# Kernel tuning notes

Measured on AMD Instinct MI355X. Metric: run time of the kernel, lower is better.

## Reference

```python
import jax, jax.numpy as jnp
import numpy as np

B = 4194304  # batch rows
DX = 10      # input feature dim (hardcoded in module)
DH = 4       # hidden dim (hardcoded in module)


def setup_inputs() -> dict:
    key = jax.random.key(0)
    ks = jax.random.split(key, 14)
    s_in = 1.0 / np.sqrt(DX)
    s_h = 1.0 / np.sqrt(DH)
    return {
        "x": jax.random.normal(ks[0], (B, DX), jnp.float32),
        "hidden": jax.random.normal(ks[1], (B, DH), jnp.float32),
        # torch.nn.Linear weights: W has shape [out, in], y = x @ W.T + b
        "Wzh": jax.random.uniform(ks[2], (DH, DH), jnp.float32, -s_h, s_h),
        "bzh": jax.random.uniform(ks[3], (DH,), jnp.float32, -s_h, s_h),
        "Wzx": jax.random.uniform(ks[4], (DH, DX), jnp.float32, -s_in, s_in),
        "bzx": jax.random.uniform(ks[5], (DH,), jnp.float32, -s_in, s_in),
        "Wrh": jax.random.uniform(ks[6], (DH, DH), jnp.float32, -s_h, s_h),
        "brh": jax.random.uniform(ks[7], (DH,), jnp.float32, -s_h, s_h),
        "Wrx": jax.random.uniform(ks[8], (DH, DX), jnp.float32, -s_in, s_in),
        "brx": jax.random.uniform(ks[9], (DH,), jnp.float32, -s_in, s_in),
        "Wnx": jax.random.uniform(ks[10], (DH, DX), jnp.float32, -s_in, s_in),
        "bnx": jax.random.uniform(ks[11], (DH,), jnp.float32, -s_in, s_in),
        "Wnh": jax.random.uniform(ks[12], (DH, DH), jnp.float32, -s_h, s_h),
        "bnh": jax.random.uniform(ks[13], (DH,), jnp.float32, -s_h, s_h),
    }


def reference(x, hidden, Wzh, bzh, Wzx, bzx, Wrh, brh, Wrx, brx, Wnx, bnx, Wnh, bnh):
    # z = sigmoid(hidden @ Wzh.T + bzh + x @ Wzx.T + bzx)
    z = jax.nn.sigmoid(hidden @ Wzh.T + bzh + x @ Wzx.T + bzx)
    r = jax.nn.sigmoid(hidden @ Wrh.T + brh + x @ Wrx.T + brx)
    n = jnp.tanh(r * (hidden @ Wnh.T + bnh) + x @ Wnx.T + bnx)
    return (1.0 - z) * n + z * hidden
```

## Files before the change

kernel.cpp:

```cpp
#include <hip/hip_runtime.h>
#include <math.h>


constexpr int DXc = 10;
constexpr int DHc = 4;

__global__ __launch_bounds__(256, 4)
void gru_fused(const float* __restrict__ x,
               const float* __restrict__ hidden,
               const float* __restrict__ Wzh, const float* __restrict__ bzh,
               const float* __restrict__ Wzx, const float* __restrict__ bzx,
               const float* __restrict__ Wrh, const float* __restrict__ brh,
               const float* __restrict__ Wrx, const float* __restrict__ brx,
               const float* __restrict__ Wnx, const float* __restrict__ bnx,
               const float* __restrict__ Wnh, const float* __restrict__ bnh,
               float* __restrict__ out, int total )
{
    const int tid = blockIdx.x * blockDim.x + threadIdx.x;
    const int nth = gridDim.x * blockDim.x;
    const int j   = tid & 3;

    float wzh[DHc], wrh[DHc], wnh[DHc];
    float wzx[DXc], wrx[DXc], wnx[DXc];
#pragma unroll
    for (int k = 0; k < DHc; ++k) {
        wzh[k] = Wzh[j * DHc + k];
        wrh[k] = Wrh[j * DHc + k];
        wnh[k] = Wnh[j * DHc + k];
    }
#pragma unroll
    for (int k = 0; k < DXc; ++k) {
        wzx[k] = Wzx[j * DXc + k];
        wrx[k] = Wrx[j * DXc + k];
        wnx[k] = Wnx[j * DXc + k];
    }
    const float bz    = bzh[j] + bzx[j];
    const float br    = brh[j] + brx[j];
    const float bnh_j = bnh[j];
    const float bnx_j = bnx[j];

    for (int p = tid; p < total; p += nth) {
        const int row = p >> 2;

        const float2* xr = reinterpret_cast<const float2*>(x + row * DXc);
        float xv[DXc];
#pragma unroll
        for (int q = 0; q < DXc / 2; ++q) {
            const float2 t = xr[q];
            xv[2 * q]     = t.x;
            xv[2 * q + 1] = t.y;
        }
        const float4 hv = *reinterpret_cast<const float4*>(hidden + row * DHc);
        const float hvv[DHc] = {hv.x, hv.y, hv.z, hv.w};

        float az = bz, ar = br, ah = bnh_j, ax = bnx_j;
#pragma unroll
        for (int k = 0; k < DHc; ++k) {
            az = fmaf(hvv[k], wzh[k], az);
            ar = fmaf(hvv[k], wrh[k], ar);
            ah = fmaf(hvv[k], wnh[k], ah);
        }
#pragma unroll
        for (int k = 0; k < DXc; ++k) {
            az = fmaf(xv[k], wzx[k], az);
            ar = fmaf(xv[k], wrx[k], ar);
            ax = fmaf(xv[k], wnx[k], ax);
        }

        const float z = 1.0f / (1.0f + expf(-az));
        const float r = 1.0f / (1.0f + expf(-ar));
        const float n = tanhf(fmaf(r, ah, ax));

        const float hj = (j < 2) ? (j == 0 ? hv.x : hv.y)
                                 : (j == 2 ? hv.z : hv.w);

        out[p] = fmaf(z, hj - n, n);
    }
}

extern "C" void kernel_launch(void* const* d_in, const int* in_sizes, int n_in,
                              void* d_out, int out_size, void* d_ws, size_t ws_size,
                              hipStream_t stream) {
    const float* x   = (const float*)d_in[0];
    const float* h   = (const float*)d_in[1];
    const float* Wzh = (const float*)d_in[2];
    const float* bzh = (const float*)d_in[3];
    const float* Wzx = (const float*)d_in[4];
    const float* bzx = (const float*)d_in[5];
    const float* Wrh = (const float*)d_in[6];
    const float* brh = (const float*)d_in[7];
    const float* Wrx = (const float*)d_in[8];
    const float* brx = (const float*)d_in[9];
    const float* Wnx = (const float*)d_in[10];
    const float* bnx = (const float*)d_in[11];
    const float* Wnh = (const float*)d_in[12];
    const float* bnh = (const float*)d_in[13];
    float* out = (float*)d_out;

    const int total = out_size;
    const int block = 256;
    const int grid  = 2048;

    gru_fused<<<grid, block, 0, stream>>>(x, h, Wzh, bzh, Wzx, bzx,
                                          Wrh, brh, Wrx, brx,
                                          Wnx, bnx, Wnh, bnh, out, total);
}
```

Baseline: 335.6 us.

## Assign one output column per wavefront with scalar weights and LDS-transposed stores

Each wavefront of a block now handles a single output column j for 64 consecutive rows. This lets all weights and biases live in scalar registers via readfirstlane, instead of every thread holding its own copy. The outputs pass through a double-buffered shared-memory transpose (with a swizzle to avoid bank conflicts) so the global store stays coalesced. Exact expf/tanhf are replaced with fast exp and hardware reciprocal, and the occupancy hint in launch bounds is raised. In exchange there is a barrier every iteration, and each row's x/hidden is now loaded by four wavefronts, relying on cache to absorb the repeats.

Result: faster. 326.5 us (-2.7%).

```diff
diff --git a/kernel.cpp b/kernel.cpp
--- a/kernel.cpp
+++ b/kernel.cpp
@@ -5,7 +5,11 @@
 constexpr int DXc = 10;
 constexpr int DHc = 4;
 
-__global__ __launch_bounds__(256, 4)
+__device__ __forceinline__ float sgpr_f(float v) {
+    return __uint_as_float(__builtin_amdgcn_readfirstlane(__float_as_uint(v)));
+}
+
+__global__ __launch_bounds__(256, 8)
 void gru_fused(const float* __restrict__ x,
                const float* __restrict__ hidden,
                const float* __restrict__ Wzh, const float* __restrict__ bzh,
@@ -14,43 +18,45 @@
                const float* __restrict__ Wrx, const float* __restrict__ brx,
                const float* __restrict__ Wnx, const float* __restrict__ bnx,
                const float* __restrict__ Wnh, const float* __restrict__ bnh,
-               float* __restrict__ out, int total )
+               float* __restrict__ out, int nrows)
 {
-    const int tid = blockIdx.x * blockDim.x + threadIdx.x;
-    const int nth = gridDim.x * blockDim.x;
-    const int j   = tid & 3;
+    __shared__ float obuf[2 * 256];
+
+    const int tid  = threadIdx.x;
+    const int lane = tid & 63;
+    const int j    = __builtin_amdgcn_readfirstlane(tid >> 6);
 
     float wzh[DHc], wrh[DHc], wnh[DHc];
     float wzx[DXc], wrx[DXc], wnx[DXc];
 #pragma unroll
     for (int k = 0; k < DHc; ++k) {
-        wzh[k] = Wzh[j * DHc + k];
-        wrh[k] = Wrh[j * DHc + k];
-        wnh[k] = Wnh[j * DHc + k];
+        wzh[k] = sgpr_f(Wzh[j * DHc + k]);
+        wrh[k] = sgpr_f(Wrh[j * DHc + k]);
+        wnh[k] = sgpr_f(Wnh[j * DHc + k]);
     }
 #pragma unroll
     for (int k = 0; k < DXc; ++k) {
-        wzx[k] = Wzx[j * DXc + k];
-        wrx[k] = Wrx[j * DXc + k];
-        wnx[k] = Wnx[j * DXc + k];
+        wzx[k] = sgpr_f(Wzx[j * DXc + k]);
+        wrx[k] = sgpr_f(Wrx[j * DXc + k]);
+        wnx[k] = sgpr_f(Wnx[j * DXc + k]);
     }
-    const float bz    = bzh[j] + bzx[j];
-    const float br    = brh[j] + brx[j];
-    const float bnh_j = bnh[j];
-    const float bnx_j = bnx[j];
+    const float bz    = sgpr_f(bzh[j] + bzx[j]);
+    const float br    = sgpr_f(brh[j] + brx[j]);
+    const float bnh_j = sgpr_f(bnh[j]);
+    const float bnx_j = sgpr_f(bnx[j]);
 
-    for (int p = tid; p < total; p += nth) {
-        const int row = p >> 2;
+    int widx = (lane << 2) | ((j + (lane >> 3)) & 3);
+    int ridx = (tid & ~3) | (((tid & 3) + (tid >> 5)) & 3);
+
+    const int rstride = gridDim.x * 64;
+    for (int row0 = blockIdx.x * 64; row0 < nrows; row0 += rstride) {
+        const int row = row0 + lane;
 
         const float2* xr = reinterpret_cast<const float2*>(x + row * DXc);
-        float xv[DXc];
-#pragma unroll
-        for (int q = 0; q < DXc / 2; ++q) {
-            const float2 t = xr[q];
-            xv[2 * q]     = t.x;
-            xv[2 * q + 1] = t.y;
-        }
+        const float2 x0 = xr[0], x1 = xr[1], x2 = xr[2], x3 = xr[3], x4 = xr[4];
         const float4 hv = *reinterpret_cast<const float4*>(hidden + row * DHc);
+        const float xv[DXc]  = {x0.x, x0.y, x1.x, x1.y, x2.x,
+                                x2.y, x3.x, x3.y, x4.x, x4.y};
         const float hvv[DHc] = {hv.x, hv.y, hv.z, hv.w};
 
         float az = bz, ar = br, ah = bnh_j, ax = bnx_j;
@@ -67,14 +73,19 @@
             ax = fmaf(xv[k], wnx[k], ax);
         }
 
-        const float z = 1.0f / (1.0f + expf(-az));
-        const float r = 1.0f / (1.0f + expf(-ar));
-        const float n = tanhf(fmaf(r, ah, ax));
+        const float z = __builtin_amdgcn_rcpf(1.0f + __expf(-az));
+        const float r = __builtin_amdgcn_rcpf(1.0f + __expf(-ar));
+        const float t = fmaf(r, ah, ax);
+        const float n = fmaf(-2.0f, __builtin_amdgcn_rcpf(1.0f + __expf(2.0f * t)), 1.0f);
 
-        const float hj = (j < 2) ? (j == 0 ? hv.x : hv.y)
-                                 : (j == 2 ? hv.z : hv.w);
+        const float hj = (j == 0) ? hv.x : (j == 1) ? hv.y : (j == 2) ? hv.z : hv.w;
+        const float o  = fmaf(z, hj - n, n);
 
-        out[p] = fmaf(z, hj - n, n);
+        obuf[widx] = o;
+        __syncthreads();
+        out[row0 * 4 + tid] = obuf[ridx];
+        widx ^= 256;
+        ridx ^= 256;
     }
 }
 
@@ -97,11 +108,11 @@
     const float* bnh = (const float*)d_in[13];
     float* out = (float*)d_out;
 
-    const int total = out_size;
+    const int nrows = out_size / 4;
     const int block = 256;
     const int grid  = 2048;
 
     gru_fused<<<grid, block, 0, stream>>>(x, h, Wzh, bzh, Wzx, bzx,
                                           Wrh, brh, Wrx, brx,
-                                          Wnx, bnx, Wnh, bnh, out, total);
+                                          Wnx, bnx, Wnh, bnh, out, nrows);
 }
```
